# Performance work log

Hardware: AMD Instinct MI355X
Metric: run time of the kernel (lower is better)

Reference implementation:

```python
import jax, jax.numpy as jnp
import numpy as np

B, T, D, H, L = 2, 1000, 768, 12, 2
DK = D // H
MLP_HID = D * 1  # mlp_ratio = 1
WIDTHS = [7, 15, 31, 63, 127, 255, 7, 15, 31, 63, 127, 255]


def _band_mask():
    # diagonal_mask(seq_len, mask_width): True = blocked (outside the diagonal band)
    i = np.arange(T)[:, None]
    j = np.arange(T)[None, :]
    m = np.stack([np.abs(i - j) > (w // 2) for w in WIDTHS], 0)  # (H, T, T)
    return jnp.asarray(m)


def _rel_pos_emb():
    # espnet-style RelPositionalEncoding: rel positions T-1 .. -(T-1), shape (2T-1, D)
    pos = jnp.arange(T - 1, -T, -1, dtype=jnp.float32)
    div = jnp.exp(jnp.arange(0, D, 2, dtype=jnp.float32) * (-np.log(10000.0) / D))
    ang = pos[:, None] * div[None, :]
    return jnp.stack([jnp.sin(ang), jnp.cos(ang)], -1).reshape(2 * T - 1, D)


def setup_inputs() -> dict:
    key = jax.random.key(0)
    ks = iter(jax.random.split(key, 32))
    rn = lambda sh, s=0.02: jax.random.normal(next(ks), sh, jnp.float32) * s
    return {
        "x": jax.random.normal(next(ks), (B, T, D), jnp.float32),
        "mask": _band_mask(),
        "ln1_g": jnp.ones((L, D)), "ln1_b": jnp.zeros((L, D)),
        "wq": rn((L, D, D)), "bq": jnp.zeros((L, D)),
        "wk": rn((L, D, D)), "bk": jnp.zeros((L, D)),
        "wv": rn((L, D, D)), "bv": jnp.zeros((L, D)),
        "wo": rn((L, D, D)), "bo": jnp.zeros((L, D)),
        "wpos": rn((L, D, D)),
        "pbu": rn((L, H, DK)), "pbv": rn((L, H, DK)),
        "ln2_g": jnp.ones((L, D)), "ln2_b": jnp.zeros((L, D)),
        "w1": rn((L, D, MLP_HID)), "b1": jnp.zeros((L, MLP_HID)),
        "w2": rn((L, MLP_HID, D)), "b2": jnp.zeros((L, D)),
    }


def _ln(x, g, b):
    m = jnp.mean(x, -1, keepdims=True)
    v = jnp.var(x, -1, keepdims=True)
    return (x - m) * jax.lax.rsqrt(v + 1e-5) * g + b


def _rel_shift(x):
    # x: (b, h, t, 2t-1) -> shifted so column s corresponds to rel pos (t-1 - s + row offset)
    b, h, t, n = x.shape
    x = jnp.pad(x, ((0, 0), (0, 0), (0, 0), (1, 0)))        # (b,h,t,2t)
    x = x.reshape(b, h, n + 1, t)[:, :, 1:, :].reshape(b, h, t, n)
    return x[..., :t]


def _forward(x, mask, p):
    (ln1_g, ln1_b, wq, bq, wk, bk, wv, bv, wo, bo,
     wpos, pbu, pbv, ln2_g, ln2_b, w1, b1, w2, b2) = p
    pe = _rel_pos_emb()                                      # (2T-1, D)
    x = x * jnp.asarray(np.sqrt(D), x.dtype)                 # xscale in RelPositionalEncoding
    neg = jnp.asarray(-1e30, x.dtype)
    inv_sqrt_dk = 1.0 / np.sqrt(DK)
    for l in range(L):
        h = _ln(x, ln1_g[l], ln1_b[l])
        q = (h @ wq[l] + bq[l]).reshape(B, T, H, DK)
        k = (h @ wk[l] + bk[l]).reshape(B, T, H, DK)
        v = (h @ wv[l] + bv[l]).reshape(B, T, H, DK)
        pp = (pe @ wpos[l]).reshape(2 * T - 1, H, DK)        # pos projection (no bias)
        ac = jnp.einsum('bthd,bshd->bhts', q + pbu[l], k)    # content term
        bd = _rel_shift(jnp.einsum('bthd,nhd->bhtn', q + pbv[l], pp))  # position term
        s = (ac + bd) * inv_sqrt_dk
        s = jnp.where(mask[None], neg, s)                    # per-head diagonal band mask
        a = jax.nn.softmax(s, axis=-1)
        o = jnp.einsum('bhts,bshd->bthd', a, v).reshape(B, T, D) @ wo[l] + bo[l]
        x = x + o
        h2 = _ln(x, ln2_g[l], ln2_b[l])
        x = x + (jax.nn.gelu(h2 @ w1[l] + b1[l], approximate=False) @ w2[l] + b2[l])
    return x


def reference(x, mask, ln1_g, ln1_b, wq, bq, wk, bk, wv, bv, wo, bo, wpos, pbu, pbv, ln2_g, ln2_b, w1, b1, w2, b2):
    return _forward(x, mask, (ln1_g, ln1_b, wq, bq, wk, bk, wv, bv, wo, bo,
                              wpos, pbu, pbv, ln2_g, ln2_b, w1, b1, w2, b2))
```

## Files before the change

### kernel.cpp

```cpp
#include <hip/hip_runtime.h>

#define TT 1000
#define BB 2
#define DD 768
#define HH 12
#define DK 64
#define LL 2
#define WELEM 589824
#define PEROWS 255
#define VTP 1312
#define LDSZ2 9216
#define PPL 195840

typedef __bf16 bf16x8 __attribute__((ext_vector_type(8)));
typedef float floatx4 __attribute__((ext_vector_type(4)));

__device__ __constant__ int HALFW[12] = {3,7,15,31,63,127,3,7,15,31,63,127};
__device__ __constant__ int HORD[12]  = {5,11,4,10,3,9,2,8,1,7,0,6};

__device__ __forceinline__ float b2f(unsigned short u){
    union { unsigned int i; float f; } x; x.i = ((unsigned int)u) << 16; return x.f;
}
__device__ __forceinline__ unsigned short f2b(float f){
    union { float f; unsigned int i; } x; x.f = f;
    unsigned int i = x.i;
    i += 0x7fffu + ((i >> 16) & 1u);
    return (unsigned short)(i >> 16);
}

__global__ __launch_bounds__(256)
void prep_kernel(const float* s0, const float* s1, const float* s2, const float* s3,
                 const float* s4, const float* s5, const float* s6,
                 unsigned short* __restrict__ dst,
                 const float* __restrict__ x, float* __restrict__ xc,
                 unsigned short* __restrict__ pe){
    int z = blockIdx.z;
    int tid = threadIdx.x;
    if (z < 14){
        const float* srcs[7] = {s0,s1,s2,s3,s4,s5,s6};
        const float* src = srcs[z % 7] + (size_t)(z / 7)*WELEM;
        unsigned short* d = dst + (size_t)z*WELEM;
        int k0 = blockIdx.x*64, n0 = blockIdx.y*64;
        __shared__ __align__(16) unsigned short tile[64][72];
        int r = tid >> 2, c = tid & 3;
        const float4* sp = (const float4*)(src + (size_t)(k0+r)*DD + n0 + c*16);
        float4 f0 = sp[0], f1 = sp[1], f2 = sp[2], f3 = sp[3];
        unsigned short u[16];
        u[0]=f2b(f0.x); u[1]=f2b(f0.y); u[2]=f2b(f0.z); u[3]=f2b(f0.w);
        u[4]=f2b(f1.x); u[5]=f2b(f1.y); u[6]=f2b(f1.z); u[7]=f2b(f1.w);
        u[8]=f2b(f2.x); u[9]=f2b(f2.y); u[10]=f2b(f2.z); u[11]=f2b(f2.w);
        u[12]=f2b(f3.x); u[13]=f2b(f3.y); u[14]=f2b(f3.z); u[15]=f2b(f3.w);
        *(int4*)&tile[r][c*16]   = *(int4*)&u[0];
        *(int4*)&tile[r][c*16+8] = *(int4*)&u[8];
        __syncthreads();
        unsigned short tmp[16];
        #pragma unroll
        for (int i=0;i<16;++i) tmp[i] = tile[c*16+i][r];
        int4* dp = (int4*)(d + (size_t)(n0+r)*DD + k0 + c*16);
        dp[0] = *(int4*)&tmp[0];
        dp[1] = *(int4*)&tmp[8];
    } else if (z == 14){
        int id = blockIdx.y*12 + blockIdx.x;
        for (int i = id*256 + tid; i < 384000; i += 36864){
            float4 v = ((const float4*)x)[i];
            v.x *= 27.712812921102035f; v.y *= 27.712812921102035f;
            v.z *= 27.712812921102035f; v.w *= 27.712812921102035f;
            ((float4*)xc)[i] = v;
        }
    } else {
        int bid = blockIdx.y*12 + blockIdx.x;
        #pragma unroll
        for (int rr = 0; rr < 2; ++rr){
            int row = bid*2 + rr;
            if (row < PEROWS){
                float pos = (float)(127 - row);
                int i = tid;
                float dv = expf((float)(2*i) * (-9.210340371976184f / 768.0f));
                float ang = pos * dv;
                pe[(size_t)row*DD + 2*i]   = f2b(sinf(ang));
                pe[(size_t)row*DD + 2*i+1] = f2b(cosf(ang));
                if (tid < 128){
                    int j = 256 + tid;
                    float dv2 = expf((float)(2*j) * (-9.210340371976184f / 768.0f));
                    float an2 = pos * dv2;
                    pe[(size_t)row*DD + 2*j]   = f2b(sinf(an2));
                    pe[(size_t)row*DD + 2*j+1] = f2b(cosf(an2));
                }
            }
        }
    }
}

__global__ __launch_bounds__(256)
void ln_kernel(const float* __restrict__ x, const float* __restrict__ g,
               const float* __restrict__ bb, unsigned short* __restrict__ out){
    int row = blockIdx.x;
    const float* xr = x + (size_t)row*DD;
    int tid = threadIdx.x;
    float v0 = xr[tid], v1 = xr[tid+256], v2 = xr[tid+512];
    float s = v0+v1+v2, ss = v0*v0+v1*v1+v2*v2;
    #pragma unroll
    for (int o=1;o<64;o<<=1){ s += __shfl_xor(s,o); ss += __shfl_xor(ss,o); }
    __shared__ float rs[4], rss[4];
    int wv = tid>>6, lane = tid&63;
    if (lane==0){ rs[wv]=s; rss[wv]=ss; }
    __syncthreads();
    s  = rs[0]+rs[1]+rs[2]+rs[3];
    ss = rss[0]+rss[1]+rss[2]+rss[3];
    float mean = s * (1.0f/768.0f);
    float var  = ss * (1.0f/768.0f) - mean*mean;
    float inv  = 1.0f / sqrtf(var + 1e-5f);
    unsigned short* orow = out + (size_t)row*DD;
    #pragma unroll
    for (int kk=0;kk<3;++kk){
        int i = tid + 256*kk;
        float v = (kk==0?v0:(kk==1?v1:v2));
        orow[i] = f2b((v - mean)*inv*g[i] + bb[i]);
    }
}

#define GEMM_PIPE64(A_, Bt_, n0_, M_)                                           \
    int tid = threadIdx.x;                                                      \
    int m0 = blockIdx.x*64;                                                     \
    int wv = tid>>6, lane = tid&63;                                             \
    int quad = lane>>4, l16 = lane&15;                                          \
    int ar = tid>>2;                                                            \
    int ac = (tid&3)*16;                                                        \
    floatx4 acc[4];                                                             \
    _Pragma("unroll")                                                           \
    for (int ni=0;ni<4;++ni) acc[ni] = (floatx4){0.f,0.f,0.f,0.f};              \
    {                                                                           \
      int r0 = m0 + ar;      if (r0 > (M_)-1) r0 = (M_)-1;                      \
      const unsigned short* Ap0 = (A_) + (size_t)r0*768 + ac;                   \
      const unsigned short* Bpp = (Bt_) + (size_t)((n0_)+ar)*768 + ac;          \
      int4 pa0 = *(const int4*)Ap0, pa1 = *(const int4*)(Ap0+8);                \
      int4 pb0 = *(const int4*)Bpp, pb1 = *(const int4*)(Bpp+8);                \
      for (int s=0; s<12; ++s){                                                 \
        unsigned short* Asb = sh + (s&1)*LDSZ2;                                 \
        unsigned short* Bsb = Asb + 4608;                                       \
        *(int4*)&Asb[ar*72 + ac]     = pa0;                                     \
        *(int4*)&Asb[ar*72 + ac + 8] = pa1;                                     \
        *(int4*)&Bsb[ar*72 + ac]     = pb0;                                     \
        *(int4*)&Bsb[ar*72 + ac + 8] = pb1;                                     \
        __syncthreads();                                                        \
        if (s < 11){                                                            \
          int off = (s+1)*64;                                                   \
          pa0 = *(const int4*)(Ap0+off); pa1 = *(const int4*)(Ap0+off+8);       \
          pb0 = *(const int4*)(Bpp+off); pb1 = *(const int4*)(Bpp+off+8);       \
        }                                                                       \
        _Pragma("unroll")                                                       \
        for (int kh=0; kh<2; ++kh){                                             \
          bf16x8 af = *(const bf16x8*)&Asb[(16*wv + l16)*72 + kh*32 + quad*8];  \
          _Pragma("unroll")                                                     \
          for (int ni=0; ni<4; ++ni){                                           \
            bf16x8 bfv = *(const bf16x8*)&Bsb[(16*ni + l16)*72 + kh*32 + quad*8]; \
            acc[ni] = __builtin_amdgcn_mfma_f32_16x16x32_bf16(af, bfv, acc[ni], 0,0,0); \
          }                                                                     \
        }                                                                       \
      }                                                                         \
    }

template<int MODE>
__global__ __launch_bounds__(256)
void gemm_kernel(const unsigned short* __restrict__ A, const unsigned short* __restrict__ Bt,
                 const float* __restrict__ bias, unsigned short* __restrict__ outb,
                 float* __restrict__ resid, int M){
    __shared__ __align__(16) unsigned short sh[2*LDSZ2];
    int n0 = blockIdx.y*64;
    int zz = blockIdx.z;
    const unsigned short* Bt_ = Bt;
    unsigned short* outb_ = outb;
    if (MODE == 3){ Bt_ = Bt + (size_t)zz*7*WELEM; outb_ = outb + (size_t)zz*PPL; }
    GEMM_PIPE64(A, Bt_, n0, M)
    float bfv_[4];
    #pragma unroll
    for (int ni=0;ni<4;++ni) bfv_[ni] = bias ? bias[n0 + 16*ni + l16] : 0.0f;
    #pragma unroll
    for (int rr=0;rr<4;++rr){
        int row = m0 + 16*wv + 4*quad + rr;
        if (row >= M) continue;
        #pragma unroll
        for (int ni=0;ni<4;++ni){
            int col = n0 + 16*ni + l16;
            float v = acc[ni][rr] + bfv_[ni];
            if (MODE == 1)      outb_[(size_t)row*768 + col] = f2b(0.5f*v*(1.0f + erff(v*0.70710678118654752f)));
            else if (MODE == 2) resid[(size_t)row*768 + col] += v;
            else {
                int h = col >> 6, d = col & 63;
                outb_[((size_t)h*PEROWS + row)*DK + d] = f2b(v);
            }
        }
    }
}

__global__ __launch_bounds__(256)
void gemm_qkv_kernel(const unsigned short* __restrict__ A, const unsigned short* __restrict__ Bt,
                     const float* __restrict__ bq, const float* __restrict__ bk, const float* __restrict__ bv,
                     unsigned short* __restrict__ qout, unsigned short* __restrict__ kout,
                     unsigned short* __restrict__ vout){
    __shared__ __align__(16) unsigned short sh[2*LDSZ2];
    int n0 = blockIdx.y*64;
    GEMM_PIPE64(A, Bt, n0, 2000)
    int sec = blockIdx.y / 12;
    int col0 = n0 - sec*768;
    int h = col0 >> 6;
    const float* bias = (sec==0) ? bq : (sec==1) ? bk : bv;
    float bfv_[4];
    #pragma unroll
    for (int ni=0;ni<4;++ni) bfv_[ni] = bias[col0 + 16*ni + l16];
    if (sec != 2){
        unsigned short* outp = (sec==0) ? qout : kout;
        #pragma unroll
        for (int rr=0;rr<4;++rr){
            int row = m0 + 16*wv + 4*quad + rr;
            if (row >= 2000) continue;
            int b = row / TT, tl = row - b*TT;
            #pragma unroll
            for (int ni=0;ni<4;++ni){
                int d = 16*ni + l16;
                outp[(((size_t)(b*HH + h))*TT + tl)*DK + d] = f2b(acc[ni][rr] + bfv_[ni]);
            }
        }
    } else {
        #pragma unroll
        for (int rr=0;rr<4;++rr){
            int rt = 16*wv + 4*quad + rr;
            #pragma unroll
            for (int ni=0;ni<4;++ni)
                sh[rt*66 + 16*ni + l16] = f2b(acc[ni][rr] + bfv_[ni]);
        }
        __syncthreads();
        #pragma unroll
        for (int it=0; it<16; ++it){
            int idx = it*256 + tid;
            int d = idx >> 6, rt = idx & 63;
            int row = m0 + rt;
            if (row < 2000){
                int b = row / TT, tl = row - b*TT;
                vout[(((size_t)(b*HH + h))*DK + d)*VTP + tl + 128] = sh[rt*66 + d];
            }
        }
    }
}

__global__ __launch_bounds__(256)
void attn_kernel(const unsigned short* __restrict__ q, const unsigned short* __restrict__ k,
                 const unsigned short* __restrict__ vT, const unsigned short* __restrict__ pp,
                 const float* __restrict__ pbu, const float* __restrict__ pbv,
                 unsigned short* __restrict__ out){
    int b = blockIdx.y, h = HORD[blockIdx.z];
    int t0 = blockIdx.x * 16;
    int w2 = HALFW[h];
    int tid = threadIdx.x;
    int wv = tid >> 6, lane = tid & 63;
    int l16 = lane & 15, quad = lane >> 4;

    const unsigned short* qB = q  + ((size_t)(b*HH + h))*TT*DK;
    const unsigned short* kB = k  + ((size_t)(b*HH + h))*TT*DK;
    const unsigned short* vB = vT + ((size_t)(b*HH + h))*DK*VTP;
    const unsigned short* pB = pp + (size_t)h*PEROWS*DK;

    __shared__ __align__(16) float bd[16*260];
    __shared__ __align__(16) unsigned short pl[16*328];
    __shared__ float mxs[4][16];
    __shared__ float sms[4][16];

    int tq = t0 + l16; if (tq > TT-1) tq = TT-1;
    union { int4 i; unsigned short u[8]; } r0, r1;
    r0.i = *(const int4*)(qB + (size_t)tq*DK + quad*8);
    r1.i = *(const int4*)(qB + (size_t)tq*DK + 32 + quad*8);
    const float* pu = pbu + h*DK + quad*8;
    const float* pv = pbv + h*DK + quad*8;
    union { unsigned short u[8]; bf16x8 v; } qu0, qu1, qv0, qv1;
    #pragma unroll
    for (int i=0;i<8;++i){
        float a0 = b2f(r0.u[i]), a1 = b2f(r1.u[i]);
        qu0.u[i] = f2b(a0 + pu[i]);
        qu1.u[i] = f2b(a1 + pu[32+i]);
        qv0.u[i] = f2b(a0 + pv[i]);
        qv1.u[i] = f2b(a1 + pv[32+i]);
    }

    int Nn = 2*w2 + 1;
    int ntiles = (Nn + 15) >> 4;
    for (int ti = wv; ti < ntiles; ti += 4){
        int n = 127 - w2 + ti*16 + l16; if (n > PEROWS-1) n = PEROWS-1;
        const unsigned short* pr = pB + (size_t)n*DK + quad*8;
        bf16x8 pb0 = *(const bf16x8*)pr;
        bf16x8 pb1 = *(const bf16x8*)(pr + 32);
        floatx4 a = {0.f,0.f,0.f,0.f};
        a = __builtin_amdgcn_mfma_f32_16x16x32_bf16(qv0.v, pb0, a, 0,0,0);
        a = __builtin_amdgcn_mfma_f32_16x16x32_bf16(qv1.v, pb1, a, 0,0,0);
        #pragma unroll
        for (int r=0;r<4;++r) bd[(quad*4+r)*260 + ti*16 + l16] = a[r];
    }
    for (int i = tid; i < 16*328/4; i += 256)
        ((unsigned long long*)pl)[i] = 0ULL;
    __syncthreads();

    int Ns = 2*w2 + 16;
    int stiles = (Ns + 15) >> 4;
    int s_lo = t0 - w2;
    float scv[5][4];
    float mx[4] = {-1e30f,-1e30f,-1e30f,-1e30f};
    #pragma unroll
    for (int ii = 0; ii < 5; ++ii){
        int ti = wv + ii*4;
        if (ti < stiles){
            int s = s_lo + ti*16 + l16;
            int sc = s < 0 ? 0 : (s > TT-1 ? TT-1 : s);
            const unsigned short* kr = kB + (size_t)sc*DK + quad*8;
            bf16x8 kb0 = *(const bf16x8*)kr;
            bf16x8 kb1 = *(const bf16x8*)(kr + 32);
            floatx4 a = {0.f,0.f,0.f,0.f};
            a = __builtin_amdgcn_mfma_f32_16x16x32_bf16(qu0.v, kb0, a, 0,0,0);
            a = __builtin_amdgcn_mfma_f32_16x16x32_bf16(qu1.v, kb1, a, 0,0,0);
            #pragma unroll
            for (int r=0;r<4;++r){
                int row = quad*4 + r;
                int nrel = ti*16 + l16 - row;
                bool ok = (nrel >= 0) && (nrel <= 2*w2) && (s >= 0) && (s <= TT-1);
                int idx = row*260 + nrel;
                idx = idx < 0 ? 0 : (idx > 16*260-1 ? 16*260-1 : idx);
                float bdv = bd[idx];
                float sc_ = ok ? (a[r] + bdv) * 0.125f : -1e30f;
                scv[ii][r] = sc_;
                mx[r] = fmaxf(mx[r], sc_);
            }
        } else {
            #pragma unroll
            for (int r=0;r<4;++r) scv[ii][r] = -1e30f;
        }
    }
    #pragma unroll
    for (int off=1; off<16; off<<=1){
        #pragma unroll
        for (int r=0;r<4;++r) mx[r] = fmaxf(mx[r], __shfl_xor(mx[r], off));
    }
    if (l16 == 0){
        #pragma unroll
        for (int r=0;r<4;++r) mxs[wv][quad*4+r] = mx[r];
    }
    __syncthreads();
    float gmx[4];
    #pragma unroll
    for (int r=0;r<4;++r){
        int row = quad*4 + r;
        gmx[r] = fmaxf(fmaxf(mxs[0][row], mxs[1][row]), fmaxf(mxs[2][row], mxs[3][row]));
    }

    int s0a = s_lo & ~31;
    int pad_lo = s_lo - s0a;
    int ktiles = (pad_lo + Ns + 31) >> 5;

    float sm[4] = {0.f,0.f,0.f,0.f};
    #pragma unroll
    for (int ii = 0; ii < 5; ++ii){
        int ti = wv + ii*4;
        if (ti < stiles){
            #pragma unroll
            for (int r=0;r<4;++r){
                float e = __expf(scv[ii][r] - gmx[r]);
                sm[r] += e;
                pl[(quad*4+r)*328 + pad_lo + ti*16 + l16] = f2b(e);
            }
        }
    }
    #pragma unroll
    for (int off=1; off<16; off<<=1){
        #pragma unroll
        for (int r=0;r<4;++r) sm[r] += __shfl_xor(sm[r], off);
    }
    if (l16 == 0){
        #pragma unroll
        for (int r=0;r<4;++r) sms[wv][quad*4+r] = sm[r];
    }
    __syncthreads();

    floatx4 oacc = {0.f,0.f,0.f,0.f};
    for (int kt = 0; kt < ktiles; ++kt){
        bf16x8 pa = *(const bf16x8*)&pl[l16*328 + kt*32 + quad*8];
        int sidx = s0a + kt*32 + quad*8 + 128;
        bf16x8 vb = *(const bf16x8*)(vB + (size_t)(wv*16 + l16)*VTP + sidx);
        oacc = __builtin_amdgcn_mfma_f32_16x16x32_bf16(pa, vb, oacc, 0,0,0);
    }
    #pragma unroll
    for (int r=0;r<4;++r){
        int row = quad*4 + r;
        float sum = sms[0][row] + sms[1][row] + sms[2][row] + sms[3][row];
        float rinv = sum > 0.f ? 1.0f/sum : 0.0f;
        int t = t0 + row;
        if (t <= TT-1)
            out[(((size_t)(b*TT + t))*HH + h)*DK + wv*16 + l16] = f2b(oacc[r] * rinv);
    }
}

extern "C" void kernel_launch(void* const* d_in, const int* in_sizes, int n_in,
                              void* d_out, int out_size, void* d_ws, size_t ws_size,
                              hipStream_t stream){
    const float* x    = (const float*)d_in[0];
    const float* ln1g = (const float*)d_in[2];
    const float* ln1b = (const float*)d_in[3];
    const float* wq   = (const float*)d_in[4];
    const float* bq   = (const float*)d_in[5];
    const float* wk   = (const float*)d_in[6];
    const float* bk   = (const float*)d_in[7];
    const float* wvv  = (const float*)d_in[8];
    const float* bv   = (const float*)d_in[9];
    const float* wo   = (const float*)d_in[10];
    const float* bo   = (const float*)d_in[11];
    const float* wpos = (const float*)d_in[12];
    const float* pbu  = (const float*)d_in[13];
    const float* pbv  = (const float*)d_in[14];
    const float* ln2g = (const float*)d_in[15];
    const float* ln2b = (const float*)d_in[16];
    const float* w1   = (const float*)d_in[17];
    const float* b1   = (const float*)d_in[18];
    const float* w2   = (const float*)d_in[19];
    const float* b2   = (const float*)d_in[20];

    const int NTOK = BB*TT;

    float* x_cur = (float*)d_out;

    char* ws = (char*)d_ws;
    unsigned short* qbuf  = (unsigned short*)(ws);
    unsigned short* kbuf  = (unsigned short*)(ws + 3072000);
    unsigned short* vTbuf = (unsigned short*)(ws + 6144000);
    unsigned short* hbuf  = (unsigned short*)(ws + 10174464);
    unsigned short* ppbuf = (unsigned short*)(ws + 13246464);
    unsigned short* pebuf = (unsigned short*)(ws + 14029824);
    unsigned short* wtbuf = (unsigned short*)(ws + 14421504);
    #define WT(t_,l_) (wtbuf + (size_t)((l_)*7 + (t_))*WELEM)

    dim3 blk(256);
    prep_kernel<<<dim3(12,12,16), blk, 0, stream>>>(wq, wk, wvv, wo, wpos, w1, w2,
                                                    wtbuf, x, x_cur, pebuf);
    gemm_kernel<3><<<dim3(4,12,2), blk, 0, stream>>>(pebuf, WT(4,0), nullptr, ppbuf, nullptr, PEROWS);

    dim3 gBig(32, 12);
    dim3 gQKV(32, 36);
    dim3 gAttn(63, BB, HH);

    for (int l = 0; l < LL; ++l){
        long dl = (long)l*DD;
        long pl_ = (long)l*HH*DK;

        ln_kernel<<<NTOK, blk, 0, stream>>>(x_cur, ln1g + dl, ln1b + dl, hbuf);
        gemm_qkv_kernel<<<gQKV, blk, 0, stream>>>(hbuf, WT(0,l), bq + dl, bk + dl, bv + dl,
                                                  qbuf, kbuf, vTbuf);

        attn_kernel<<<gAttn, blk, 0, stream>>>(qbuf, kbuf, vTbuf, ppbuf + (size_t)l*PPL,
                                               pbu + pl_, pbv + pl_, hbuf);

        gemm_kernel<2><<<gBig, blk, 0, stream>>>(hbuf, WT(3,l), bo + dl, nullptr, x_cur, NTOK);

        ln_kernel<<<NTOK, blk, 0, stream>>>(x_cur, ln2g + dl, ln2b + dl, hbuf);
        gemm_kernel<1><<<gBig, blk, 0, stream>>>(hbuf, WT(5,l), b1 + dl, qbuf, nullptr, NTOK);
        gemm_kernel<2><<<gBig, blk, 0, stream>>>(qbuf, WT(6,l), b2 + dl, nullptr, x_cur, NTOK);
    }
}
```

Baseline: 314.6 us.

## Enlarge GEMM M-tile to 128 rows with two MFMA row fragments per wave

Adds a 128-row GEMM pipeline in which each wave computes two 16-row MFMA fragments that share the same B fragment loads. It is used for the QKV, output-projection and MLP GEMMs, which halves the block count along M. The positional-projection GEMM is split into its own kernel that keeps the old 64-row path. The aim is to halve B-tile traffic and LDS reads per output. The cost is fewer blocks (192 for the square GEMMs on a chip with many CUs), higher register and LDS use, and possibly lower occupancy.

```diff
diff --git a/kernel.cpp b/kernel.cpp
--- a/kernel.cpp
+++ b/kernel.cpp
@@ -10,6 +10,7 @@
 #define PEROWS 255
 #define VTP 1312
 #define LDSZ2 9216
+#define LDSB128 13824
 #define PPL 195840
 
 typedef __bf16 bf16x8 __attribute__((ext_vector_type(8)));
@@ -160,35 +161,104 @@
       }                                                                         \
     }
 
+#define GEMM_PIPE128(A_, Bt_, n0_, M_)                                          \
+    int tid = threadIdx.x;                                                      \
+    int m0 = blockIdx.x*128;                                                    \
+    int wv = tid>>6, lane = tid&63;                                             \
+    int quad = lane>>4, l16 = lane&15;                                          \
+    int ar = tid>>2;                                                            \
+    int ac = (tid&3)*16;                                                        \
+    floatx4 acc[2][4];                                                          \
+    _Pragma("unroll")                                                           \
+    for (int hf=0;hf<2;++hf){                                                   \
+      _Pragma("unroll")                                                         \
+      for (int ni=0;ni<4;++ni) acc[hf][ni] = (floatx4){0.f,0.f,0.f,0.f};        \
+    }                                                                           \
+    {                                                                           \
+      int r0 = m0 + ar;       if (r0 > (M_)-1) r0 = (M_)-1;                     \
+      int r1 = m0 + ar + 64;  if (r1 > (M_)-1) r1 = (M_)-1;                     \
+      const unsigned short* Ap0 = (A_) + (size_t)r0*768 + ac;                   \
+      const unsigned short* Ap1 = (A_) + (size_t)r1*768 + ac;                   \
+      const unsigned short* Bpp = (Bt_) + (size_t)((n0_)+ar)*768 + ac;          \
+      int4 pa0 = *(const int4*)Ap0, pa1 = *(const int4*)(Ap0+8);                \
+      int4 pa2 = *(const int4*)Ap1, pa3 = *(const int4*)(Ap1+8);                \
+      int4 pb0 = *(const int4*)Bpp, pb1 = *(const int4*)(Bpp+8);                \
+      for (int s=0; s<12; ++s){                                                 \
+        unsigned short* Asb = sh + (s&1)*LDSB128;                               \
+        unsigned short* Bsb = Asb + 9216;                                       \
+        *(int4*)&Asb[ar*72 + ac]          = pa0;                                \
+        *(int4*)&Asb[ar*72 + ac + 8]      = pa1;                                \
+        *(int4*)&Asb[(ar+64)*72 + ac]     = pa2;                                \
+        *(int4*)&Asb[(ar+64)*72 + ac + 8] = pa3;                                \
+        *(int4*)&Bsb[ar*72 + ac]          = pb0;                                \
+        *(int4*)&Bsb[ar*72 + ac + 8]      = pb1;                                \
+        __syncthreads();                                                        \
+        if (s < 11){                                                            \
+          int off = (s+1)*64;                                                   \
+          pa0 = *(const int4*)(Ap0+off); pa1 = *(const int4*)(Ap0+off+8);       \
+          pa2 = *(const int4*)(Ap1+off); pa3 = *(const int4*)(Ap1+off+8);       \
+          pb0 = *(const int4*)(Bpp+off); pb1 = *(const int4*)(Bpp+off+8);       \
+        }                                                                       \
+        _Pragma("unroll")                                                       \
+        for (int kh=0; kh<2; ++kh){                                             \
+          bf16x8 af0 = *(const bf16x8*)&Asb[(32*wv + l16)*72 + kh*32 + quad*8]; \
+          bf16x8 af1 = *(const bf16x8*)&Asb[(32*wv + 16 + l16)*72 + kh*32 + quad*8]; \
+          _Pragma("unroll")                                                     \
+          for (int ni=0; ni<4; ++ni){                                           \
+            bf16x8 bfv = *(const bf16x8*)&Bsb[(16*ni + l16)*72 + kh*32 + quad*8]; \
+            acc[0][ni] = __builtin_amdgcn_mfma_f32_16x16x32_bf16(af0, bfv, acc[0][ni], 0,0,0); \
+            acc[1][ni] = __builtin_amdgcn_mfma_f32_16x16x32_bf16(af1, bfv, acc[1][ni], 0,0,0); \
+          }                                                                     \
+        }                                                                       \
+      }                                                                         \
+    }
+
 template<int MODE>
 __global__ __launch_bounds__(256)
 void gemm_kernel(const unsigned short* __restrict__ A, const unsigned short* __restrict__ Bt,
                  const float* __restrict__ bias, unsigned short* __restrict__ outb,
                  float* __restrict__ resid, int M){
+    __shared__ __align__(16) unsigned short sh[2*LDSB128];
+    int n0 = blockIdx.y*64;
+    GEMM_PIPE128(A, Bt, n0, M)
+    float bfv_[4];
+    #pragma unroll
+    for (int ni=0;ni<4;++ni) bfv_[ni] = bias ? bias[n0 + 16*ni + l16] : 0.0f;
+    #pragma unroll
+    for (int hf=0;hf<2;++hf){
+        #pragma unroll
+        for (int rr=0;rr<4;++rr){
+            int row = m0 + 32*wv + hf*16 + 4*quad + rr;
+            if (row >= M) continue;
+            #pragma unroll
+            for (int ni=0;ni<4;++ni){
+                int col = n0 + 16*ni + l16;
+                float v = acc[hf][ni][rr] + bfv_[ni];
+                if (MODE == 1)      outb[(size_t)row*768 + col] = f2b(0.5f*v*(1.0f + erff(v*0.70710678118654752f)));
+                else                resid[(size_t)row*768 + col] += v;
+            }
+        }
+    }
+}
+
+__global__ __launch_bounds__(256)
+void gemm_pos_kernel(const unsigned short* __restrict__ A, const unsigned short* __restrict__ Bt,
+                     unsigned short* __restrict__ outb){
     __shared__ __align__(16) unsigned short sh[2*LDSZ2];
     int n0 = blockIdx.y*64;
     int zz = blockIdx.z;
-    const unsigned short* Bt_ = Bt;
-    unsigned short* outb_ = outb;
-    if (MODE == 3){ Bt_ = Bt + (size_t)zz*7*WELEM; outb_ = outb + (size_t)zz*PPL; }
-    GEMM_PIPE64(A, Bt_, n0, M)
-    float bfv_[4];
-    #pragma unroll
-    for (int ni=0;ni<4;++ni) bfv_[ni] = bias ? bias[n0 + 16*ni + l16] : 0.0f;
+    const unsigned short* Bt_ = Bt + (size_t)zz*7*WELEM;
+    unsigned short* outb_ = outb + (size_t)zz*PPL;
+    GEMM_PIPE64(A, Bt_, n0, PEROWS)
     #pragma unroll
     for (int rr=0;rr<4;++rr){
         int row = m0 + 16*wv + 4*quad + rr;
-        if (row >= M) continue;
+        if (row >= PEROWS) continue;
         #pragma unroll
         for (int ni=0;ni<4;++ni){
             int col = n0 + 16*ni + l16;
-            float v = acc[ni][rr] + bfv_[ni];
-            if (MODE == 1)      outb_[(size_t)row*768 + col] = f2b(0.5f*v*(1.0f + erff(v*0.70710678118654752f)));
-            else if (MODE == 2) resid[(size_t)row*768 + col] += v;
-            else {
-                int h = col >> 6, d = col & 63;
-                outb_[((size_t)h*PEROWS + row)*DK + d] = f2b(v);
-            }
+            int h = col >> 6, d = col & 63;
+            outb_[((size_t)h*PEROWS + row)*DK + d] = f2b(acc[ni][rr]);
         }
     }
 }
@@ -198,9 +268,9 @@
                      const float* __restrict__ bq, const float* __restrict__ bk, const float* __restrict__ bv,
                      unsigned short* __restrict__ qout, unsigned short* __restrict__ kout,
                      unsigned short* __restrict__ vout){
-    __shared__ __align__(16) unsigned short sh[2*LDSZ2];
+    __shared__ __align__(16) unsigned short sh[2*LDSB128];
     int n0 = blockIdx.y*64;
-    GEMM_PIPE64(A, Bt, n0, 2000)
+    GEMM_PIPE128(A, Bt, n0, 2000)
     int sec = blockIdx.y / 12;
     int col0 = n0 - sec*768;
     int h = col0 >> 6;
@@ -211,29 +281,35 @@
     if (sec != 2){
         unsigned short* outp = (sec==0) ? qout : kout;
         #pragma unroll
-        for (int rr=0;rr<4;++rr){
-            int row = m0 + 16*wv + 4*quad + rr;
-            if (row >= 2000) continue;
-            int b = row / TT, tl = row - b*TT;
+        for (int hf=0;hf<2;++hf){
             #pragma unroll
-            for (int ni=0;ni<4;++ni){
-                int d = 16*ni + l16;
-                outp[(((size_t)(b*HH + h))*TT + tl)*DK + d] = f2b(acc[ni][rr] + bfv_[ni]);
+            for (int rr=0;rr<4;++rr){
+                int row = m0 + 32*wv + hf*16 + 4*quad + rr;
+                if (row >= 2000) continue;
+                int b = row / TT, tl = row - b*TT;
+                #pragma unroll
+                for (int ni=0;ni<4;++ni){
+                    int d = 16*ni + l16;
+                    outp[(((size_t)(b*HH + h))*TT + tl)*DK + d] = f2b(acc[hf][ni][rr] + bfv_[ni]);
+                }
             }
         }
     } else {
         #pragma unroll
-        for (int rr=0;rr<4;++rr){
-            int rt = 16*wv + 4*quad + rr;
+        for (int hf=0;hf<2;++hf){
             #pragma unroll
-            for (int ni=0;ni<4;++ni)
-                sh[rt*66 + 16*ni + l16] = f2b(acc[ni][rr] + bfv_[ni]);
+            for (int rr=0;rr<4;++rr){
+                int rt = 32*wv + hf*16 + 4*quad + rr;
+                #pragma unroll
+                for (int ni=0;ni<4;++ni)
+                    sh[rt*66 + 16*ni + l16] = f2b(acc[hf][ni][rr] + bfv_[ni]);
+            }
         }
         __syncthreads();
         #pragma unroll
-        for (int it=0; it<16; ++it){
+        for (int it=0; it<32; ++it){
             int idx = it*256 + tid;
-            int d = idx >> 6, rt = idx & 63;
+            int d = idx >> 7, rt = idx & 127;
             int row = m0 + rt;
             if (row < 2000){
                 int b = row / TT, tl = row - b*TT;
@@ -436,10 +512,10 @@
     dim3 blk(256);
     prep_kernel<<<dim3(12,12,16), blk, 0, stream>>>(wq, wk, wvv, wo, wpos, w1, w2,
                                                     wtbuf, x, x_cur, pebuf);
-    gemm_kernel<3><<<dim3(4,12,2), blk, 0, stream>>>(pebuf, WT(4,0), nullptr, ppbuf, nullptr, PEROWS);
-
-    dim3 gBig(32, 12);
-    dim3 gQKV(32, 36);
+    gemm_pos_kernel<<<dim3(4,12,2), blk, 0, stream>>>(pebuf, WT(4,0), ppbuf);
+
+    dim3 gBig(16, 12);
+    dim3 gQKV(16, 36);
     dim3 gAttn(63, BB, HH);
 
     for (int l = 0; l < LL; ++l){
```

After: 337.8 us. +7.4%, slower.

## Load GEMM tiles directly to LDS with global_load_lds and XOR swizzle

Applied to the files above, without the earlier changes.

Rewrites the shared GEMM mainloop so global tiles go straight into LDS via the global_load_lds builtin instead of passing through registers. The padded 72-wide layout is replaced by an XOR-swizzled 64-wide layout to avoid bank conflicts, and the sync moves to the end of each k-step. This cuts register pressure and VALU store instructions in the load path. The positional-projection GEMM is split into its own kernel so the mode dispatch is simpler.

```diff
diff --git a/kernel.cpp b/kernel.cpp
--- a/kernel.cpp
+++ b/kernel.cpp
@@ -9,7 +9,6 @@
 #define WELEM 589824
 #define PEROWS 255
 #define VTP 1312
-#define LDSZ2 9216
 #define PPL 195840
 
 typedef __bf16 bf16x8 __attribute__((ext_vector_type(8)));
@@ -26,6 +25,11 @@
     unsigned int i = x.i;
     i += 0x7fffu + ((i >> 16) & 1u);
     return (unsigned short)(i >> 16);
+}
+__device__ __forceinline__ void gload16(const void* g, void* l){
+    __builtin_amdgcn_global_load_lds(
+        (const __attribute__((address_space(1))) void*)g,
+        (__attribute__((address_space(3))) void*)l, 16, 0, 0);
 }
 
 __global__ __launch_bounds__(256)
@@ -119,44 +123,57 @@
     }
 }
 
-#define GEMM_PIPE64(A_, Bt_, n0_, M_)                                           \
+#define GEMM_GL64(A_, Bt_, n0_, M_)                                             \
     int tid = threadIdx.x;                                                      \
     int m0 = blockIdx.x*64;                                                     \
     int wv = tid>>6, lane = tid&63;                                             \
     int quad = lane>>4, l16 = lane&15;                                          \
-    int ar = tid>>2;                                                            \
-    int ac = (tid&3)*16;                                                        \
     floatx4 acc[4];                                                             \
     _Pragma("unroll")                                                           \
     for (int ni=0;ni<4;++ni) acc[ni] = (floatx4){0.f,0.f,0.f,0.f};              \
     {                                                                           \
-      int r0 = m0 + ar;      if (r0 > (M_)-1) r0 = (M_)-1;                      \
-      const unsigned short* Ap0 = (A_) + (size_t)r0*768 + ac;                   \
-      const unsigned short* Bpp = (Bt_) + (size_t)((n0_)+ar)*768 + ac;          \
-      int4 pa0 = *(const int4*)Ap0, pa1 = *(const int4*)(Ap0+8);                \
-      int4 pb0 = *(const int4*)Bpp, pb1 = *(const int4*)(Bpp+8);                \
+      int rl0 = wv*16 + (lane>>3);                                              \
+      int rl1 = rl0 + 8;                                                        \
+      int gc  = (lane&7) ^ (lane>>3);                                           \
+      int ra0 = m0 + rl0; if (ra0 > (M_)-1) ra0 = (M_)-1;                       \
+      int ra1 = m0 + rl1; if (ra1 > (M_)-1) ra1 = (M_)-1;                       \
+      const char* gA0 = (const char*)(A_)  + (size_t)ra0*1536 + gc*16;          \
+      const char* gA1 = (const char*)(A_)  + (size_t)ra1*1536 + gc*16;          \
+      const char* gB0 = (const char*)(Bt_) + (size_t)((n0_)+rl0)*1536 + gc*16;  \
+      const char* gB1 = (const char*)(Bt_) + (size_t)((n0_)+rl1)*1536 + gc*16;  \
+      char* shB = (char*)sh;                                                    \
+      int ld0 = (2*wv)*1024, ld1 = (2*wv+1)*1024;                               \
+      int arow = (16*wv + l16)*64;                                              \
+      int sw8  = l16 & 7;                                                       \
+      int cq0 = (quad ^ sw8)*8;                                                 \
+      int cq1 = ((4|quad) ^ sw8)*8;                                             \
+      gload16(gA0, shB + ld0);                                                  \
+      gload16(gA1, shB + ld1);                                                  \
+      gload16(gB0, shB + 8192 + ld0);                                           \
+      gload16(gB1, shB + 8192 + ld1);                                           \
+      __syncthreads();                                                          \
       for (int s=0; s<12; ++s){                                                 \
-        unsigned short* Asb = sh + (s&1)*LDSZ2;                                 \
-        unsigned short* Bsb = Asb + 4608;                                       \
-        *(int4*)&Asb[ar*72 + ac]     = pa0;                                     \
-        *(int4*)&Asb[ar*72 + ac + 8] = pa1;                                     \
-        *(int4*)&Bsb[ar*72 + ac]     = pb0;                                     \
-        *(int4*)&Bsb[ar*72 + ac + 8] = pb1;                                     \
-        __syncthreads();                                                        \
         if (s < 11){                                                            \
-          int off = (s+1)*64;                                                   \
-          pa0 = *(const int4*)(Ap0+off); pa1 = *(const int4*)(Ap0+off+8);       \
-          pb0 = *(const int4*)(Bpp+off); pb1 = *(const int4*)(Bpp+off+8);       \
+          char* nb = shB + ((s+1)&1)*16384;                                     \
+          int off = (s+1)*128;                                                  \
+          gload16(gA0 + off, nb + ld0);                                         \
+          gload16(gA1 + off, nb + ld1);                                         \
+          gload16(gB0 + off, nb + 8192 + ld0);                                  \
+          gload16(gB1 + off, nb + 8192 + ld1);                                  \
         }                                                                       \
+        const unsigned short* cA = sh + (s&1)*8192;                             \
+        const unsigned short* cB = cA + 4096;                                   \
         _Pragma("unroll")                                                       \
         for (int kh=0; kh<2; ++kh){                                             \
-          bf16x8 af = *(const bf16x8*)&Asb[(16*wv + l16)*72 + kh*32 + quad*8];  \
+          int cq = kh ? cq1 : cq0;                                              \
+          bf16x8 af = *(const bf16x8*)&cA[arow + cq];                           \
           _Pragma("unroll")                                                     \
           for (int ni=0; ni<4; ++ni){                                           \
-            bf16x8 bfv = *(const bf16x8*)&Bsb[(16*ni + l16)*72 + kh*32 + quad*8]; \
+            bf16x8 bfv = *(const bf16x8*)&cB[ni*1024 + l16*64 + cq];            \
             acc[ni] = __builtin_amdgcn_mfma_f32_16x16x32_bf16(af, bfv, acc[ni], 0,0,0); \
           }                                                                     \
         }                                                                       \
+        __syncthreads();                                                        \
       }                                                                         \
     }
 
@@ -165,13 +182,9 @@
 void gemm_kernel(const unsigned short* __restrict__ A, const unsigned short* __restrict__ Bt,
                  const float* __restrict__ bias, unsigned short* __restrict__ outb,
                  float* __restrict__ resid, int M){
-    __shared__ __align__(16) unsigned short sh[2*LDSZ2];
+    __shared__ __align__(16) unsigned short sh[16384];
     int n0 = blockIdx.y*64;
-    int zz = blockIdx.z;
-    const unsigned short* Bt_ = Bt;
-    unsigned short* outb_ = outb;
-    if (MODE == 3){ Bt_ = Bt + (size_t)zz*7*WELEM; outb_ = outb + (size_t)zz*PPL; }
-    GEMM_PIPE64(A, Bt_, n0, M)
+    GEMM_GL64(A, Bt, n0, M)
     float bfv_[4];
     #pragma unroll
     for (int ni=0;ni<4;++ni) bfv_[ni] = bias ? bias[n0 + 16*ni + l16] : 0.0f;
@@ -183,12 +196,30 @@
         for (int ni=0;ni<4;++ni){
             int col = n0 + 16*ni + l16;
             float v = acc[ni][rr] + bfv_[ni];
-            if (MODE == 1)      outb_[(size_t)row*768 + col] = f2b(0.5f*v*(1.0f + erff(v*0.70710678118654752f)));
-            else if (MODE == 2) resid[(size_t)row*768 + col] += v;
-            else {
-                int h = col >> 6, d = col & 63;
-                outb_[((size_t)h*PEROWS + row)*DK + d] = f2b(v);
-            }
+            if (MODE == 1)      outb[(size_t)row*768 + col] = f2b(0.5f*v*(1.0f + erff(v*0.70710678118654752f)));
+            else                resid[(size_t)row*768 + col] += v;
+        }
+    }
+}
+
+__global__ __launch_bounds__(256)
+void gemm_pos_kernel(const unsigned short* __restrict__ A, const unsigned short* __restrict__ Bt,
+                     unsigned short* __restrict__ outb){
+    __shared__ __align__(16) unsigned short sh[16384];
+    int n0 = blockIdx.y*64;
+    int zz = blockIdx.z;
+    const unsigned short* Bt_ = Bt + (size_t)zz*7*WELEM;
+    unsigned short* outb_ = outb + (size_t)zz*PPL;
+    GEMM_GL64(A, Bt_, n0, PEROWS)
+    #pragma unroll
+    for (int rr=0;rr<4;++rr){
+        int row = m0 + 16*wv + 4*quad + rr;
+        if (row >= PEROWS) continue;
+        #pragma unroll
+        for (int ni=0;ni<4;++ni){
+            int col = n0 + 16*ni + l16;
+            int h = col >> 6, d = col & 63;
+            outb_[((size_t)h*PEROWS + row)*DK + d] = f2b(acc[ni][rr]);
         }
     }
 }
@@ -198,9 +229,9 @@
                      const float* __restrict__ bq, const float* __restrict__ bk, const float* __restrict__ bv,
                      unsigned short* __restrict__ qout, unsigned short* __restrict__ kout,
                      unsigned short* __restrict__ vout){
-    __shared__ __align__(16) unsigned short sh[2*LDSZ2];
+    __shared__ __align__(16) unsigned short sh[16384];
     int n0 = blockIdx.y*64;
-    GEMM_PIPE64(A, Bt, n0, 2000)
+    GEMM_GL64(A, Bt, n0, 2000)
     int sec = blockIdx.y / 12;
     int col0 = n0 - sec*768;
     int h = col0 >> 6;
@@ -436,7 +467,7 @@
     dim3 blk(256);
     prep_kernel<<<dim3(12,12,16), blk, 0, stream>>>(wq, wk, wvv, wo, wpos, w1, w2,
                                                     wtbuf, x, x_cur, pebuf);
-    gemm_kernel<3><<<dim3(4,12,2), blk, 0, stream>>>(pebuf, WT(4,0), nullptr, ppbuf, nullptr, PEROWS);
+    gemm_pos_kernel<<<dim3(4,12,2), blk, 0, stream>>>(pebuf, WT(4,0), ppbuf);
 
     dim3 gBig(32, 12);
     dim3 gQKV(32, 36);
```

After: 293.5 us. -6.7%, faster.
